# Optimization experiments

Hardware: AMD Instinct MI355X
Metric: run time of the kernel (lower is better)

The kernel has to match this reference:

```python
import jax, jax.numpy as jnp
import numpy as np

N = 4096
LAT, COND, PH, E = 64, 219, 20, 8
H, OUT = 512, 171
GIN = PH * 2 + LAT  # 104


def setup_inputs() -> dict:
    key = jax.random.key(0)
    ks = jax.random.split(key, 15)
    s = 0.05  # small init scale for stability under ELU/softmax
    return {
        "latent": jax.random.normal(ks[0], (N, LAT), jnp.float32),
        "condition": jax.random.normal(ks[1], (N, COND), jnp.float32),
        "phase": jax.random.normal(ks[2], (N, PH, 2), jnp.float32),
        "gate_w1": jax.random.normal(ks[3], (GIN, 128), jnp.float32) * s,
        "gate_b1": jnp.zeros((128,), jnp.float32),
        "gate_w2": jax.random.normal(ks[4], (128, 128), jnp.float32) * s,
        "gate_b2": jnp.zeros((128,), jnp.float32),
        "gate_w3": jax.random.normal(ks[5], (128, E), jnp.float32) * s,
        "gate_b3": jnp.zeros((E,), jnp.float32),
        "w0": jax.random.normal(ks[6], (E, COND + LAT, H), jnp.float32) * s,
        "b0": jnp.zeros((E, H), jnp.float32),
        "w1": jax.random.normal(ks[7], (E, H + LAT, H), jnp.float32) * s,
        "b1": jnp.zeros((E, H), jnp.float32),
        "w2": jax.random.normal(ks[8], (E, H, OUT), jnp.float32) * s,
        "b2": jnp.zeros((E, OUT), jnp.float32),
    }


def _moe_linear(x, coeff, W, b):
    # Per-sample expert blend: out_n = sum_e coeff[n,e] * (x_n @ W[e] + b[e])
    # (mathematically identical to blending weights first, but avoids
    #  materializing an [N, in, out] per-sample weight tensor)
    h = jnp.einsum('ni,eio->neo', x, W) + b[None]  # [N, E, out]
    return jnp.einsum('ne,neo->no', coeff, h)


def reference(latent, condition, phase,
              gate_w1, gate_b1, gate_w2, gate_b2, gate_w3, gate_b3,
              w0, b0, w1, b1, w2, b2):
    elu = jax.nn.elu
    # gate network: softmax over experts
    g = jnp.concatenate([phase.reshape(phase.shape[0], -1), latent], axis=-1)
    g = elu(g @ gate_w1 + gate_b1)
    g = elu(g @ gate_w2 + gate_b2)
    coeff = jax.nn.softmax(g @ gate_w3 + gate_b3, axis=-1)  # [N, E]
    # expert-blended MLP with latent re-concatenation
    x = jnp.concatenate([condition, latent], axis=-1)
    x = elu(_moe_linear(x, coeff, w0, b0))
    x = jnp.concatenate([x, latent], axis=-1)
    x = elu(_moe_linear(x, coeff, w1, b1))
    pred_pose = _moe_linear(x, coeff, w2, b2)
    return pred_pose, coeff
```

## Files before the change

### kernel.cpp

```cpp
#include <hip/hip_runtime.h>
#include <hip/hip_bf16.h>

#define NR 4096

typedef float f32x4 __attribute__((ext_vector_type(4)));
typedef __bf16 bf16x8 __attribute__((ext_vector_type(8)));

typedef __attribute__((address_space(1))) unsigned int u32_g;
typedef __attribute__((address_space(3))) unsigned int u32_l;

__device__ __forceinline__ void gl_lds16(const void* g, void* l) {
  __builtin_amdgcn_global_load_lds((const u32_g*)g, (u32_l*)l, 16, 0, 0);
}


__device__ void wstage2p(const float* __restrict__ w, __hip_bfloat16* __restrict__ out,
                         int Kin, int KT, int Oin, int u, char* LDS)
{
  int ob = u / (KT * 2);
  int rem = u - ob * (KT * 2);
  int T = rem >> 1, s = rem & 1;
  float* t = (float*)LDS;
  const int tid = threadIdx.x;
  const int kbase = T * 64 + s * 32;
  const size_t segbase = (((size_t)ob * KT + T) * 2 + s) * 16384;

#pragma unroll 1
  for (int h = 0; h < 2; ++h) {
    if (Oin == 512) {
#pragma unroll
      for (int i = 0; i < 4; ++i) {
        int idx = i * 256 + tid;
        int row = idx >> 3, c4 = idx & 7;
        int e = h * 4 + (row >> 5), kk = row & 31;
        int k = kbase + kk;
        float4 v = {0.f, 0.f, 0.f, 0.f};
        if (k < Kin) v = *(const float4*)&w[((size_t)e * Kin + k) * 512 + ob * 32 + c4 * 4];
        t[row * 33 + c4 * 4 + 0] = v.x;
        t[row * 33 + c4 * 4 + 1] = v.y;
        t[row * 33 + c4 * 4 + 2] = v.z;
        t[row * 33 + c4 * 4 + 3] = v.w;
      }
    } else {
#pragma unroll
      for (int i = 0; i < 4; ++i) {
        int idx = i * 256 + tid;
        int row = idx >> 3, c4 = idx & 7;
        int e = h * 4 + (row >> 5), kk = row & 31;
        int k = kbase + kk;
#pragma unroll
        for (int j = 0; j < 4; ++j) {
          int o = ob * 32 + c4 * 4 + j;
          float f = (k < Kin && o < Oin) ? w[((size_t)e * Kin + k) * (size_t)Oin + o] : 0.f;
          t[row * 33 + c4 * 4 + j] = f;
        }
      }
    }
    __syncthreads();
    if (tid < 128) {
      int p = ((tid >> 5) << 6) | (h << 5) | (tid & 31);
      int e = ((p >> 4) & 3) * 2 + (p & 1);
      int oo = ((p >> 6) & 3) * 8 + ((p >> 1) & 7);
#pragma unroll
      for (int g = 0; g < 4; ++g) {
        bf16x8 v;
#pragma unroll
        for (int e8 = 0; e8 < 8; ++e8)
          v[e8] = (__bf16)t[((e & 3) * 32 + g * 8 + e8) * 33 + oo];
        *(bf16x8*)((char*)out + segbase + g * 4096 + (size_t)p * 16) = v;
      }
    }
    __syncthreads();
  }
}

__device__ void x0stage16(int u, const float* __restrict__ cond, const float* __restrict__ lat,
                          __hip_bfloat16* __restrict__ out, char* LDS)
{
  float* Lc = (float*)LDS;
  float* Ll = (float*)(LDS + 14144);
  const int tid = threadIdx.x;
  const int n0 = u * 16;

  for (int i = tid; i < 16 * 219; i += 256) {
    int r = i / 219, c = i - r * 219;
    Lc[r * 221 + c] = cond[(size_t)n0 * 219 + i];
  }
  for (int i = tid; i < 16 * 64; i += 256) {
    int r = i >> 6, c = i & 63;
    Ll[r * 65 + c] = lat[(size_t)n0 * 64 + i];
  }
  __syncthreads();

  const int RB = u >> 4;
  const int rbase = (u & 15) * 16;
#pragma unroll
  for (int ii = 0; ii < 3; ++ii) {
    int cc = ii * 256 + tid;
    if (cc < 640) {
      int row = cc & 15, kc = cc >> 4;
      int T = kc >> 3, s = (kc >> 2) & 1, g = kc & 3;
      bf16x8 v;
#pragma unroll
      for (int j = 0; j < 8; ++j) {
        int k = kc * 8 + j;
        float f = (k < 219) ? Lc[row * 221 + k]
                : (k < 283) ? Ll[row * 65 + (k - 219)] : 0.f;
        v[j] = (__bf16)f;
      }
      size_t off = (((size_t)RB * 5 + T) * 2 + s) * 16384 + (size_t)g * 4096
                 + (size_t)(rbase + row) * 16;
      *(bf16x8*)((char*)out + off) = v;
    }
  }
}

__device__ void x1stage64(int u, const float* __restrict__ lat,
                          __hip_bfloat16* __restrict__ out, char* LDS)
{
  float* L = (float*)LDS;
  const int tid = threadIdx.x;
  const int n0 = u * 64;
  for (int i = tid; i < 64 * 64; i += 256) {
    int r = i >> 6, c = i & 63;
    L[r * 65 + c] = lat[(size_t)n0 * 64 + i];
  }
  __syncthreads();
  const int RB = u >> 2;
  const int rbase = (u & 3) * 64;
#pragma unroll
  for (int ii = 0; ii < 2; ++ii) {
    int cc = ii * 256 + tid;
    int row = cc & 63, kc = cc >> 6;
    int s = kc >> 2, g = kc & 3;
    bf16x8 v;
#pragma unroll
    for (int j = 0; j < 8; ++j) v[j] = (__bf16)L[row * 65 + kc * 8 + j];
    size_t off = ((size_t)RB * 9 + 8) * 32768
               + (size_t)((s << 10) | (g << 8) | (rbase + row)) * 16;
    *(bf16x8*)((char*)out + off) = v;
  }
}

__device__ void gate8(int gb, const float* __restrict__ phs, const float* __restrict__ lat,
                      const float* __restrict__ gw1, const float* __restrict__ gb1,
                      const float* __restrict__ gw2, const float* __restrict__ gb2,
                      const float* __restrict__ gw3, const float* __restrict__ gb3,
                      float* __restrict__ coeff, char* LDS)
{
  float* aT  = (float*)LDS;
  float* h1T = (float*)(LDS + 4096);
  float* w3L = (float*)(LDS + 8192);
  const int tid = threadIdx.x;
  const int n0 = gb * 8;

  for (int i = tid; i < 104 * 8; i += 256) {
    int k = i >> 3, r = i & 7;
    aT[i] = (k < 40) ? phs[(size_t)(n0 + r) * 40 + k]
                     : lat[(size_t)(n0 + r) * 64 + (k - 40)];
  }
  ((float4*)w3L)[tid] = ((const float4*)gw3)[tid];
  __syncthreads();

  const int col = tid & 127, rh = tid >> 7;
  {
    f32x4 acc = {};
#pragma unroll 8
    for (int k = 0; k < 104; ++k) {
      float w = gw1[k * 128 + col];
      f32x4 g4 = *(const f32x4*)&aT[k * 8 + rh * 4];
      acc += g4 * w;
    }
    float bb = gb1[col];
    f32x4 v = acc + bb;
#pragma unroll
    for (int j = 0; j < 4; ++j) v[j] = v[j] > 0.f ? v[j] : expm1f(v[j]);
    *(f32x4*)&h1T[col * 8 + rh * 4] = v;
  }
  __syncthreads();
  {
    f32x4 acc = {};
#pragma unroll 8
    for (int k = 0; k < 128; ++k) {
      float w = gw2[k * 128 + col];
      f32x4 g4 = *(const f32x4*)&h1T[k * 8 + rh * 4];
      acc += g4 * w;
    }
    float bb = gb2[col];
    f32x4 v = acc + bb;
#pragma unroll
    for (int j = 0; j < 4; ++j) v[j] = v[j] > 0.f ? v[j] : expm1f(v[j]);
    *(f32x4*)&aT[col * 8 + rh * 4] = v;
  }
  __syncthreads();
  if (tid < 64) {
    int row = tid >> 3, e = tid & 7;
    float a3 = 0.f;
#pragma unroll 8
    for (int k = 0; k < 128; ++k) a3 += aT[k * 8 + row] * w3L[k * 8 + e];
    float lgt = a3 + gb3[e];
    float m = lgt;
    m = fmaxf(m, __shfl_xor(m, 1));
    m = fmaxf(m, __shfl_xor(m, 2));
    m = fmaxf(m, __shfl_xor(m, 4));
    float ex = expf(lgt - m);
    float s = ex;
    s += __shfl_xor(s, 1);
    s += __shfl_xor(s, 2);
    s += __shfl_xor(s, 4);
    coeff[(size_t)(n0 + row) * 8 + e] = ex / s;
  }
}

__global__ __launch_bounds__(256) void prepG(
    const float* __restrict__ latent, const float* __restrict__ condition,
    const float* __restrict__ phase,
    const float* __restrict__ gw1, const float* __restrict__ gb1,
    const float* __restrict__ gw2, const float* __restrict__ gb2,
    const float* __restrict__ gw3, const float* __restrict__ gb3,
    const float* __restrict__ w0, const float* __restrict__ w1, const float* __restrict__ w2,
    __hip_bfloat16* x0s, __hip_bfloat16* x1s,
    __hip_bfloat16* w0s, __hip_bfloat16* w1s, __hip_bfloat16* w2s,
    float* coeff)
{
  __shared__ __align__(16) char LDS[18432];
  int b = blockIdx.x;
  if (b < 512) {
    gate8(b, phase, latent, gw1, gb1, gw2, gb2, gw3, gb3, coeff, LDS);
    return;
  }
  b -= 512;
  if (b < 288)       wstage2p(w1, w1s, 576, 9, 512, b, LDS);
  else if (b < 448)  wstage2p(w0, w0s, 283, 5, 512, b - 288, LDS);
  else if (b < 544)  wstage2p(w2, w2s, 512, 8, 171, b - 448, LDS);
  else if (b < 800)  x0stage16(b - 544, condition, latent, x0s, LDS);
  else               x1stage64(b - 800, latent, x1s, LDS);
}

template <int KT, int KTD, int MODE, int BYPG>
__global__ __launch_bounds__(512, 4) void gemm_k(
    const __hip_bfloat16* __restrict__ Ap, const __hip_bfloat16* __restrict__ Bp,
    const float* __restrict__ coeff, const float* __restrict__ bias,
    __hip_bfloat16* __restrict__ dstS, float* __restrict__ dstF)
{
  __shared__ __align__(16) char lds[49152];
  const int bid = blockIdx.x;
  const int xcd = bid & 7, r = bid >> 3;
  const int bx = ((xcd & 3) << 3) + (r & 7);
  const int by = (xcd >> 2) * BYPG + (r >> 3);
  const int tid = threadIdx.x;
  const int lane = tid & 63;
  const int wid = tid >> 6;
  const int wr = wid >> 2, wc = wid & 3;
  const int l15 = lane & 15, lg = lane >> 4;
  const int aHalf = (bx & 1) * 2048;

  const char* aG = (const char*)Ap + (size_t)(bx >> 1) * KT * 32768;
  const char* bG = (const char*)Bp + (size_t)by * KT * 32768;

#define STAGE(T)                                                             \
  {                                                                          \
    const char* gA_ = aG + (size_t)(T) * 32768;                              \
    const char* gB_ = bG + (size_t)(T) * 32768;                              \
    _Pragma("unroll") for (int i = 0; i < 2; ++i) {                          \
      int c = i * 512 + tid;                                                 \
      gl_lds16(gA_ + (c >> 9) * 16384 + ((c >> 7) & 3) * 4096 + aHalf        \
                   + (c & 127) * 16,                                         \
               lds + c * 16);                                                \
    }                                                                        \
    _Pragma("unroll") for (int i = 0; i < 4; ++i) {                          \
      int c = i * 512 + tid;                                                 \
      gl_lds16(gB_ + c * 16, lds + 16384 + c * 16);                          \
    }                                                                        \
  }

  f32x4 acc[4][4] = {};

  STAGE(0);
  asm volatile("s_waitcnt vmcnt(0)" ::: "memory");
  __builtin_amdgcn_s_barrier();

#pragma unroll 1
  for (int t = 0; t < KT; ++t) {
#pragma unroll
    for (int s = 0; s < 2; ++s) {
      bf16x8 a[4], b[4];
#pragma unroll
      for (int fm = 0; fm < 4; ++fm)
        a[fm] = *(const bf16x8*)(lds + s * 8192 + lg * 2048
                                 + ((wr << 6) + fm * 16 + l15) * 16);
#pragma unroll
      for (int nf = 0; nf < 4; ++nf)
        b[nf] = *(const bf16x8*)(lds + 16384 + s * 16384 + lg * 4096
                                 + (wc << 10) + nf * 256 + l15 * 16);
#pragma unroll
      for (int fm = 0; fm < 4; ++fm)
#pragma unroll
        for (int nf = 0; nf < 4; ++nf)
          acc[fm][nf] = __builtin_amdgcn_mfma_f32_16x16x32_bf16(a[fm], b[nf], acc[fm][nf], 0, 0, 0);
    }
    if (t + 1 < KT) {
      __builtin_amdgcn_s_barrier();
      STAGE(t + 1);
      asm volatile("s_waitcnt vmcnt(0)" ::: "memory");
      __builtin_amdgcn_s_barrier();
    }
  }
#undef STAGE
  __syncthreads();

  float* cl2 = (float*)lds;
  float* tb  = (float*)(lds + 4352);
  {
#pragma unroll
    for (int i = 0; i < 2; ++i) {
      int idx = i * 512 + tid;
      int e = idx & 7, n = idx >> 3;
      cl2[e * 132 + n] = coeff[((size_t)bx * 128 + n) * 8 + e];
    }
  }
  __syncthreads();
  const int e0 = lane & 1;
  const int o_loc = (wc << 3) + (l15 >> 1);

  if (MODE == 0) {
    float bb[4];
#pragma unroll
    for (int fn = 0; fn < 4; ++fn) bb[fn] = bias[(fn * 2 + e0) * 512 + by * 32 + o_loc];
#pragma unroll
    for (int fm = 0; fm < 4; ++fm) {
#pragma unroll
      for (int r2 = 0; r2 < 4; ++r2) {
        int n_loc = (wr << 6) + fm * 16 + (lg << 2) + r2;
        float s = 0.f;
#pragma unroll
        for (int fn = 0; fn < 4; ++fn)
          s += cl2[(fn * 2 + e0) * 132 + n_loc] * (acc[fm][fn][r2] + bb[fn]);
        s += __shfl_xor(s, 1);
        s = s > 0.f ? s : expm1f(s);
        if ((lane & 1) == (fm & 1)) tb[n_loc * 33 + o_loc] = s;
      }
    }
    __syncthreads();
    {
      int n_loc = tid & 127, c = tid >> 7;
      const float* p = &tb[n_loc * 33 + c * 8];
      bf16x8 v;
#pragma unroll
      for (int j = 0; j < 8; ++j) v[j] = (__bf16)p[j];
      size_t off = (((size_t)(bx >> 1) * KTD + (by >> 1)) * 2 + (by & 1)) * 16384
                 + (size_t)c * 4096 + (size_t)((bx & 1) * 128 + n_loc) * 16;
      *(bf16x8*)((char*)dstS + off) = v;
    }
  } else {
    const int o_g = by * 32 + o_loc;
    if (o_g < 171) {
      float bb[4];
#pragma unroll
      for (int fn = 0; fn < 4; ++fn) bb[fn] = bias[(fn * 2 + e0) * 171 + o_g];
#pragma unroll
      for (int fm = 0; fm < 4; ++fm) {
#pragma unroll
        for (int r2 = 0; r2 < 4; ++r2) {
          int n_loc = (wr << 6) + fm * 16 + (lg << 2) + r2;
          float s = 0.f;
#pragma unroll
          for (int fn = 0; fn < 4; ++fn)
            s += cl2[(fn * 2 + e0) * 132 + n_loc] * (acc[fm][fn][r2] + bb[fn]);
          s += __shfl_xor(s, 1);
          if ((lane & 1) == (fm & 1))
            dstF[(size_t)(bx * 128 + n_loc) * 171 + o_g] = s;
        }
      }
    }
  }
}

extern "C" void kernel_launch(void* const* d_in, const int* in_sizes, int n_in,
                              void* d_out, int out_size, void* d_ws, size_t ws_size,
                              hipStream_t stream)
{
  const float* latent    = (const float*)d_in[0];
  const float* condition = (const float*)d_in[1];
  const float* phase     = (const float*)d_in[2];
  const float* gw1 = (const float*)d_in[3];
  const float* gb1 = (const float*)d_in[4];
  const float* gw2 = (const float*)d_in[5];
  const float* gb2 = (const float*)d_in[6];
  const float* gw3 = (const float*)d_in[7];
  const float* gb3 = (const float*)d_in[8];
  const float* w0  = (const float*)d_in[9];
  const float* b0  = (const float*)d_in[10];
  const float* w1  = (const float*)d_in[11];
  const float* b1  = (const float*)d_in[12];
  const float* w2  = (const float*)d_in[13];
  const float* b2  = (const float*)d_in[14];

  float* out   = (float*)d_out;
  float* coeff = out + (size_t)NR * 171;

  char* ws = (char*)d_ws;
  __hip_bfloat16* x0s = (__hip_bfloat16*)ws; ws += (size_t)16 * 5 * 32768;
  __hip_bfloat16* x1s = (__hip_bfloat16*)ws; ws += (size_t)16 * 9 * 32768;
  __hip_bfloat16* x2s = (__hip_bfloat16*)ws; ws += (size_t)16 * 8 * 32768;
  __hip_bfloat16* w0s = (__hip_bfloat16*)ws; ws += (size_t)16 * 5 * 32768;
  __hip_bfloat16* w1s = (__hip_bfloat16*)ws; ws += (size_t)16 * 9 * 32768;
  __hip_bfloat16* w2s = (__hip_bfloat16*)ws; ws += (size_t)6 * 8 * 32768;

  prepG<<<1376, 256, 0, stream>>>(latent, condition, phase,
                                  gw1, gb1, gw2, gb2, gw3, gb3,
                                  w0, w1, w2,
                                  x0s, x1s, w0s, w1s, w2s, coeff);

  gemm_k<5, 9, 0, 8><<<512, 512, 0, stream>>>(x0s, w0s, coeff, b0, x1s, nullptr);
  gemm_k<9, 8, 0, 8><<<512, 512, 0, stream>>>(x1s, w1s, coeff, b1, x2s, nullptr);
  gemm_k<8, 0, 1, 3><<<192, 512, 0, stream>>>(x2s, w2s, coeff, b2, nullptr, out);
}
```

Baseline: 70.29 us.

## Halve GEMM tile width and double-buffer LDS stages with 256-thread blocks

The GEMM kernels switch from 512-thread blocks with a 128x256 (8-expert×32-out) tile to 256-thread blocks covering half the output columns, doubling the grid. The single LDS stage is replaced by two 32KB buffers so the global-to-LDS load of tile t+2 overlaps compute on tile t, waiting only on older loads. The epilogue index math is reworked for the half-width tile. This trades more blocks and more A-tile reloads for better latency hiding and more parallelism, and the 64KB LDS footprint may limit blocks per CU.

After: 77.11 us. +9.7%, slower.

```diff
diff --git a/kernel.cpp b/kernel.cpp
--- a/kernel.cpp
+++ b/kernel.cpp
@@ -238,12 +238,12 @@
 }
 
 template <int KT, int KTD, int MODE, int BYPG>
-__global__ __launch_bounds__(512, 4) void gemm_k(
+__global__ __launch_bounds__(256, 2) void gemm_k(
     const __hip_bfloat16* __restrict__ Ap, const __hip_bfloat16* __restrict__ Bp,
     const float* __restrict__ coeff, const float* __restrict__ bias,
     __hip_bfloat16* __restrict__ dstS, float* __restrict__ dstF)
 {
-  __shared__ __align__(16) char lds[49152];
+  __shared__ __align__(16) char lds[65536];
   const int bid = blockIdx.x;
   const int xcd = bid & 7, r = bid >> 3;
   const int bx = ((xcd & 3) << 3) + (r & 7);
@@ -251,48 +251,53 @@
   const int tid = threadIdx.x;
   const int lane = tid & 63;
   const int wid = tid >> 6;
-  const int wr = wid >> 2, wc = wid & 3;
+  const int wr = wid >> 1, wc = wid & 1;
   const int l15 = lane & 15, lg = lane >> 4;
   const int aHalf = (bx & 1) * 2048;
+  const int bHalf = (by & 1) * 2048;
 
   const char* aG = (const char*)Ap + (size_t)(bx >> 1) * KT * 32768;
-  const char* bG = (const char*)Bp + (size_t)by * KT * 32768;
-
-#define STAGE(T)                                                             \
+  const char* bG = (const char*)Bp + (size_t)(by >> 1) * KT * 32768;
+
+#define STAGE(T, L)                                                          \
   {                                                                          \
     const char* gA_ = aG + (size_t)(T) * 32768;                              \
     const char* gB_ = bG + (size_t)(T) * 32768;                              \
-    _Pragma("unroll") for (int i = 0; i < 2; ++i) {                          \
-      int c = i * 512 + tid;                                                 \
+    _Pragma("unroll") for (int i = 0; i < 4; ++i) {                          \
+      int c = i * 256 + tid;                                                 \
       gl_lds16(gA_ + (c >> 9) * 16384 + ((c >> 7) & 3) * 4096 + aHalf        \
                    + (c & 127) * 16,                                         \
-               lds + c * 16);                                                \
+               (L) + c * 16);                                                \
     }                                                                        \
     _Pragma("unroll") for (int i = 0; i < 4; ++i) {                          \
-      int c = i * 512 + tid;                                                 \
-      gl_lds16(gB_ + c * 16, lds + 16384 + c * 16);                          \
+      int c = i * 256 + tid;                                                 \
+      gl_lds16(gB_ + (c >> 9) * 16384 + ((c >> 7) & 3) * 4096 + bHalf        \
+                   + (c & 127) * 16,                                         \
+               (L) + 16384 + c * 16);                                        \
     }                                                                        \
   }
 
   f32x4 acc[4][4] = {};
 
-  STAGE(0);
-  asm volatile("s_waitcnt vmcnt(0)" ::: "memory");
+  STAGE(0, lds);
+  STAGE(1, lds + 32768);
+  asm volatile("s_waitcnt vmcnt(8)" ::: "memory");
   __builtin_amdgcn_s_barrier();
 
 #pragma unroll 1
   for (int t = 0; t < KT; ++t) {
+    char* cL = lds + ((t & 1) << 15);
 #pragma unroll
     for (int s = 0; s < 2; ++s) {
       bf16x8 a[4], b[4];
 #pragma unroll
       for (int fm = 0; fm < 4; ++fm)
-        a[fm] = *(const bf16x8*)(lds + s * 8192 + lg * 2048
+        a[fm] = *(const bf16x8*)(cL + s * 8192 + lg * 2048
                                  + ((wr << 6) + fm * 16 + l15) * 16);
 #pragma unroll
       for (int nf = 0; nf < 4; ++nf)
-        b[nf] = *(const bf16x8*)(lds + 16384 + s * 16384 + lg * 4096
-                                 + (wc << 10) + nf * 256 + l15 * 16);
+        b[nf] = *(const bf16x8*)(cL + 16384 + s * 8192 + lg * 2048
+                                 + ((wc << 6) + nf * 16 + l15) * 16);
 #pragma unroll
       for (int fm = 0; fm < 4; ++fm)
 #pragma unroll
@@ -301,8 +306,12 @@
     }
     if (t + 1 < KT) {
       __builtin_amdgcn_s_barrier();
-      STAGE(t + 1);
-      asm volatile("s_waitcnt vmcnt(0)" ::: "memory");
+      if (t + 2 < KT) {
+        STAGE(t + 2, cL);
+        asm volatile("s_waitcnt vmcnt(8)" ::: "memory");
+      } else {
+        asm volatile("s_waitcnt vmcnt(0)" ::: "memory");
+      }
       __builtin_amdgcn_s_barrier();
     }
   }
@@ -313,20 +322,21 @@
   float* tb  = (float*)(lds + 4352);
   {
 #pragma unroll
-    for (int i = 0; i < 2; ++i) {
-      int idx = i * 512 + tid;
+    for (int i = 0; i < 4; ++i) {
+      int idx = i * 256 + tid;
       int e = idx & 7, n = idx >> 3;
       cl2[e * 132 + n] = coeff[((size_t)bx * 128 + n) * 8 + e];
     }
   }
   __syncthreads();
   const int e0 = lane & 1;
-  const int o_loc = (wc << 3) + (l15 >> 1);
+  const int o_tb = (wc << 3) + (l15 >> 1);
+  const int o_g = (by >> 1) * 32 + (by & 1) * 16 + o_tb;
 
   if (MODE == 0) {
     float bb[4];
 #pragma unroll
-    for (int fn = 0; fn < 4; ++fn) bb[fn] = bias[(fn * 2 + e0) * 512 + by * 32 + o_loc];
+    for (int nf = 0; nf < 4; ++nf) bb[nf] = bias[(nf * 2 + e0) * 512 + o_g];
 #pragma unroll
     for (int fm = 0; fm < 4; ++fm) {
 #pragma unroll
@@ -334,30 +344,31 @@
         int n_loc = (wr << 6) + fm * 16 + (lg << 2) + r2;
         float s = 0.f;
 #pragma unroll
-        for (int fn = 0; fn < 4; ++fn)
-          s += cl2[(fn * 2 + e0) * 132 + n_loc] * (acc[fm][fn][r2] + bb[fn]);
+        for (int nf = 0; nf < 4; ++nf)
+          s += cl2[(nf * 2 + e0) * 132 + n_loc] * (acc[fm][nf][r2] + bb[nf]);
         s += __shfl_xor(s, 1);
         s = s > 0.f ? s : expm1f(s);
-        if ((lane & 1) == (fm & 1)) tb[n_loc * 33 + o_loc] = s;
+        if ((lane & 1) == (fm & 1)) tb[n_loc * 17 + o_tb] = s;
       }
     }
     __syncthreads();
     {
-      int n_loc = tid & 127, c = tid >> 7;
-      const float* p = &tb[n_loc * 33 + c * 8];
+      int n_loc = tid & 127, oc = tid >> 7;
+      int k_g = (by >> 1) * 32 + (by & 1) * 16 + oc * 8;
+      const float* p = &tb[n_loc * 17 + oc * 8];
       bf16x8 v;
 #pragma unroll
       for (int j = 0; j < 8; ++j) v[j] = (__bf16)p[j];
-      size_t off = (((size_t)(bx >> 1) * KTD + (by >> 1)) * 2 + (by & 1)) * 16384
-                 + (size_t)c * 4096 + (size_t)((bx & 1) * 128 + n_loc) * 16;
+      int T = k_g >> 6, s2 = (k_g >> 5) & 1, g2 = (k_g >> 3) & 3;
+      size_t off = (((size_t)(bx >> 1) * KTD + T) * 2 + s2) * 16384
+                 + (size_t)g2 * 4096 + (size_t)((bx & 1) * 128 + n_loc) * 16;
       *(bf16x8*)((char*)dstS + off) = v;
     }
   } else {
-    const int o_g = by * 32 + o_loc;
     if (o_g < 171) {
       float bb[4];
 #pragma unroll
-      for (int fn = 0; fn < 4; ++fn) bb[fn] = bias[(fn * 2 + e0) * 171 + o_g];
+      for (int nf = 0; nf < 4; ++nf) bb[nf] = bias[(nf * 2 + e0) * 171 + o_g];
 #pragma unroll
       for (int fm = 0; fm < 4; ++fm) {
 #pragma unroll
@@ -365,8 +376,8 @@
           int n_loc = (wr << 6) + fm * 16 + (lg << 2) + r2;
           float s = 0.f;
 #pragma unroll
-          for (int fn = 0; fn < 4; ++fn)
-            s += cl2[(fn * 2 + e0) * 132 + n_loc] * (acc[fm][fn][r2] + bb[fn]);
+          for (int nf = 0; nf < 4; ++nf)
+            s += cl2[(nf * 2 + e0) * 132 + n_loc] * (acc[fm][nf][r2] + bb[nf]);
           s += __shfl_xor(s, 1);
           if ((lane & 1) == (fm & 1))
             dstF[(size_t)(bx * 128 + n_loc) * 171 + o_g] = s;
@@ -412,7 +423,7 @@
                                   w0, w1, w2,
                                   x0s, x1s, w0s, w1s, w2s, coeff);
 
-  gemm_k<5, 9, 0, 8><<<512, 512, 0, stream>>>(x0s, w0s, coeff, b0, x1s, nullptr);
-  gemm_k<9, 8, 0, 8><<<512, 512, 0, stream>>>(x1s, w1s, coeff, b1, x2s, nullptr);
-  gemm_k<8, 0, 1, 3><<<192, 512, 0, stream>>>(x2s, w2s, coeff, b2, nullptr, out);
-}
+  gemm_k<5, 9, 0, 16><<<1024, 256, 0, stream>>>(x0s, w0s, coeff, b0, x1s, nullptr);
+  gemm_k<9, 8, 0, 16><<<1024, 256, 0, stream>>>(x1s, w1s, coeff, b1, x2s, nullptr);
+  gemm_k<8, 0, 1, 6><<<384, 256, 0, stream>>>(x2s, w2s, coeff, b2, nullptr, out);
+}
```
